# Performance work log

Hardware: AMD Instinct MI355X
Metric: run time of the kernel (lower is better)

## Reference

```python
import jax, jax.numpy as jnp
import numpy as np
from functools import partial

B, L, V = 64, 512, 20000
P, M = 150, 6          # total patterns, max pattern length
NEG = -1e9             # semiring zero (log-space)
END_STATES = np.repeat(np.array([3, 4, 5]), 50)  # pattern_len-1 per pattern


@jax.custom_vjp
def ste_heaviside(x):
    return (x > 0).astype(x.dtype)

def _ste_fwd(x):
    return ste_heaviside(x), None

def _ste_bwd(_, g):
    return (g,)  # straight-through identity (matches torch code path)

ste_heaviside.defvjp(_ste_fwd, _ste_bwd)


def setup_inputs() -> dict:
    key = jax.random.key(0)
    ks = jax.random.split(key, 8)
    return {
        "docs": jax.random.randint(ks[0], (B, L), 0, V),
        "doc_lens": jax.random.randint(ks[1], (B,), 1, L),
        "local_embeddings": jax.random.normal(ks[2], (300, V), jnp.float32),
        "diags": jax.random.normal(ks[3], (P * M, 300), jnp.float32) * 0.05,
        "bias": jax.random.normal(ks[4], (P * M, 1), jnp.float32) * 0.05,
        "wildcards": jax.random.normal(ks[5], (P, M - 1), jnp.float32) * 0.05,
        "ln_gamma": jnp.ones((P,), jnp.float32),
        "ln_beta": jnp.zeros((P,), jnp.float32),
        "linear_w": jax.random.normal(ks[6], (2, P), jnp.float32) * 0.05,
        "linear_b": jnp.zeros((2,), jnp.float32),
    }


def reference(docs, doc_lens, local_embeddings, diags, bias, wildcards,
              ln_gamma, ln_beta, linear_w, linear_b):
    end_states = jnp.asarray(END_STATES)                  # [P]
    pat_idx = jnp.arange(P)

    # transition matrices over local vocab, mapped into log-space semiring
    tm_vocab = jax.nn.log_sigmoid((diags @ local_embeddings + bias).T)  # [V, P*M]
    tm = tm_vocab[docs].reshape(B, L, P, M)               # [B,L,P,M]

    # wildcard transitions: semiring.times(one=0, log_sigmoid(wildcards))
    wild = jax.nn.log_sigmoid(wildcards)                  # [P, M-1]

    restart = jnp.zeros((B, P, 1), tm.dtype)              # semiring one
    hid0 = jnp.full((B, P, M), NEG, tm.dtype).at[:, :, 0].set(0.0)
    scores0 = jnp.full((B, P), NEG, tm.dtype)             # semiring zero

    def step(carry, inputs):
        hid, sc = carry
        t, tm_t = inputs                                  # tm_t: [B,P,M]
        main = jnp.concatenate([restart, hid[:, :, :-1] + tm_t[:, :, :-1]], axis=2)
        wildp = jnp.concatenate([restart, hid[:, :, :-1] + wild[None]], axis=2)
        hid = jnp.maximum(main, wildp)                    # semiring plus
        esv = hid[:, pat_idx, end_states]                 # [B,P]
        active = (doc_lens > t)[:, None]
        sc = jnp.where(active, jnp.maximum(sc, esv), sc)
        return (hid, sc), None

    xs = (jnp.arange(L), jnp.moveaxis(tm, 1, 0))          # [L], [L,B,P,M]
    (_, scores), _ = jax.lax.scan(step, (hid0, scores0), xs)

    scores = jnp.exp(scores)                              # from_semiring_to_outer
    mu = scores.mean(axis=-1, keepdims=True)
    var = scores.var(axis=-1, keepdims=True)
    norm = (scores - mu) * jax.lax.rsqrt(var + 1e-5) * ln_gamma + ln_beta
    binar = ste_heaviside(norm)
    return binar @ linear_w.T + linear_b
```

## Files before the change

### kernel.cpp

```cpp
#include <hip/hip_runtime.h>
#include <hip/hip_bf16.h>
#include <hip/hip_fp16.h>
#include <math.h>

#define B_   64
#define L_   512
#define V_   20000
#define P_   150
#define M_   6
#define KDIM 300
#define NOUT 750
#define CWS  752
#define NEGF (-1.0e9f)

#define BM 128
#define BN 128
#define BK 16
#define LDP 132

#define KP 320
#define NIT 10
#define NVG 157
#define NJ  6
#define TILE_U4 1024
#define SA 1024.0f
#define SB 16384.0f
#define INV24 (5.9604644775390625e-8f)

#define TCHUNK 32
#define NCHUNK (L_ / TCHUNK)
#define WARM   5
#define CS_STRIDE 160

typedef _Float16 f16x8 __attribute__((ext_vector_type(8)));
typedef float f32x16 __attribute__((ext_vector_type(16)));

__device__ __forceinline__ float logsigf(float x) {
    return fminf(x, 0.f) - log1pf(expf(-fabsf(x)));
}

__device__ __forceinline__ float logsigf_fast(float x) {
    return fminf(x, 0.f) - __logf(1.f + __expf(-fabsf(x)));
}

__device__ __forceinline__ void gload_lds16(const void* gp, void* lp) {
    __builtin_amdgcn_global_load_lds(
        (const __attribute__((address_space(1))) unsigned int*)gp,
        (__attribute__((address_space(3))) unsigned int*)lp, 16, 0, 0);
}


__global__ __launch_bounds__(256) void p12_split(
    const float* __restrict__ emb, const float* __restrict__ diags,
    uint4* __restrict__ a_t, uint4* __restrict__ b_t)
{
    __shared__ float T[64][132];
    const int t   = threadIdx.x;
    const int bid = blockIdx.x;

    if (bid < NVG * 5) {
        const int gx = bid % NVG;
        const int ky = bid / NVG;
        const int v0 = gx * 128;
        const int k0 = ky * 64;

        #pragma unroll
        for (int pass = 0; pass < 8; ++pass) {
            int flat = pass * 256 + t;
            int krow = flat >> 5;
            int c4   = (flat & 31) * 4;
            int kg   = k0 + krow;
            int v    = v0 + c4;
            float4 f = {0.f, 0.f, 0.f, 0.f};
            if (kg < KDIM && v + 3 < V_)
                f = *(const float4*)(emb + (size_t)kg * V_ + v);
            *(float4*)&T[krow][c4] = f;
        }
        __syncthreads();

        const int vv = t >> 1;
        const int kh = (t & 1) * 32;
        const int it = ky * 2 + (kh >> 5);
        const int v  = v0 + vv;
        if (v < V_) {
            union { ushort u[8]; uint4 q; } H[4], Lo[4];
            #pragma unroll
            for (int i = 0; i < 32; ++i) {
                float x = T[kh + i][vv] * SA;
                __half h = __float2half_rn(x);
                float rem = x - __half2float(h);
                H[i >> 3].u[i & 7]  = __half_as_ushort(h);
                Lo[i >> 3].u[i & 7] = __half_as_ushort(__float2half_rn(rem));
            }
            uint4* tile = a_t + ((size_t)gx * NIT + it) * TILE_U4;
            #pragma unroll
            for (int c = 0; c < 4; ++c) {
                tile[      c * 128 + vv] = H[c].q;
                tile[512 + c * 128 + vv] = Lo[c].q;
            }
        }
    } else {
        const int bidx = bid - NVG * 5;
        const int it   = bidx % NIT;
        const int j    = bidx / NIT;
        const int row  = t >> 1;
        const int qh   = (t & 1) * 2;
        const int n    = j * 128 + row;
        const bool nok = (n < NOUT);
        const int pm   = nok ? ((n / 5) * 6 + (n % 5)) : 0;
        uint4* tile = b_t + (size_t)bidx * TILE_U4;
        #pragma unroll
        for (int qq = 0; qq < 2; ++qq) {
            int q = qh + qq;
            union { ushort u[8]; uint4 v; } H, Lo;
            #pragma unroll
            for (int e = 0; e < 8; ++e) {
                int k = it * 32 + q * 8 + e;
                float x = (nok && k < KDIM) ? diags[(size_t)pm * KDIM + k] * SB : 0.f;
                __half h = __float2half_rn(x);
                float rem = x - __half2float(h);
                H.u[e]  = __half_as_ushort(h);
                Lo.u[e] = __half_as_ushort(__float2half_rn(rem));
            }
            tile[      q * 128 + row] = H.v;
            tile[512 + q * 128 + row] = Lo.v;
        }
    }
}

__global__ __launch_bounds__(256, 2) void k1m_gemm(
    const uint4* __restrict__ a_t, const uint4* __restrict__ b_t,
    const float* __restrict__ bias, const float* __restrict__ wildc,
    float* __restrict__ cw)
{
    const int bid  = blockIdx.x;
    const int xcd  = bid & 7;
    const int slot = bid >> 3;
    const int g    = xcd + 8 * (slot / 6);
    const int j    = slot % 6;
    if (g >= NVG) return;

    __shared__ uint4 sm[2][2048];
    const int t    = threadIdx.x;
    const int lane = t & 63;
    const int w    = t >> 6;
    const int wr   = w >> 1, wc = w & 1;
    const int v0   = g * 128;
    const int n0   = j * 128;

    const uint4* gsec = (w < 2)
        ? a_t + (size_t)g * NIT * TILE_U4 + w * 512
        : b_t + (size_t)j * NIT * TILE_U4 + (w - 2) * 512;

    const int fk16 = lane >> 5;
    const int fm   = lane & 31;

    f32x16 acc[2][2];
    #pragma unroll
    for (int i = 0; i < 2; ++i)
        #pragma unroll
        for (int jj = 0; jj < 2; ++jj)
            #pragma unroll
            for (int r = 0; r < 16; ++r) acc[i][jj][r] = 0.f;

    {
        const uint4* gp = gsec + lane;
        #pragma unroll
        for (int i = 0; i < 8; ++i)
            gload_lds16(gp + i * 64, &sm[0][w * 512 + i * 64 + lane]);
    }

    int cur = 0;
    for (int it = 0; it < NIT; ++it) {
        __syncthreads();

        if (it + 1 < NIT) {
            const uint4* gp = gsec + (size_t)(it + 1) * TILE_U4 + lane;
            #pragma unroll
            for (int i = 0; i < 8; ++i)
                gload_lds16(gp + i * 64, &sm[cur ^ 1][w * 512 + i * 64 + lane]);
        }

        const uint4* smc = sm[cur];
        #pragma unroll
        for (int s = 0; s < 2; ++s) {
            f16x8 A1[2], A2[2], B1[2], B2[2];
            const int q = s * 2 + fk16;
            #pragma unroll
            for (int ri = 0; ri < 2; ++ri) {
                A1[ri] = *(const f16x8*)&smc[(0 * 4 + q) * 128 + wr * 64 + ri * 32 + fm];
                A2[ri] = *(const f16x8*)&smc[(1 * 4 + q) * 128 + wr * 64 + ri * 32 + fm];
            }
            #pragma unroll
            for (int cj = 0; cj < 2; ++cj) {
                B1[cj] = *(const f16x8*)&smc[(2 * 4 + q) * 128 + wc * 64 + cj * 32 + fm];
                B2[cj] = *(const f16x8*)&smc[(3 * 4 + q) * 128 + wc * 64 + cj * 32 + fm];
            }
            #pragma unroll
            for (int ri = 0; ri < 2; ++ri)
                #pragma unroll
                for (int cj = 0; cj < 2; ++cj) {
                    acc[ri][cj] = __builtin_amdgcn_mfma_f32_32x32x16_f16(A1[ri], B1[cj], acc[ri][cj], 0, 0, 0);
                    acc[ri][cj] = __builtin_amdgcn_mfma_f32_32x32x16_f16(A1[ri], B2[cj], acc[ri][cj], 0, 0, 0);
                    acc[ri][cj] = __builtin_amdgcn_mfma_f32_32x32x16_f16(A2[ri], B1[cj], acc[ri][cj], 0, 0, 0);
                }
        }
        cur ^= 1;
    }

    float biasv[2], lwv[2]; int ncol[2]; bool nok[2];
    #pragma unroll
    for (int cj = 0; cj < 2; ++cj) {
        int n = n0 + wc * 64 + cj * 32 + fm;
        ncol[cj] = n;
        nok[cj]  = (n < NOUT);
        int nc = nok[cj] ? n : 0;
        int pm = (nc / 5) * 6 + (nc % 5);
        biasv[cj] = bias[pm];
        lwv[cj]   = logsigf_fast(wildc[nc]);
    }
    #pragma unroll
    for (int ri = 0; ri < 2; ++ri) {
        int vbase = v0 + wr * 64 + ri * 32 + 4 * fk16;
        #pragma unroll
        for (int cj = 0; cj < 2; ++cj) {
            if (!nok[cj]) continue;
            #pragma unroll
            for (int r = 0; r < 16; ++r) {
                int v = vbase + (r & 3) + 8 * (r >> 2);
                if (v < V_) {
                    float val = acc[ri][cj][r] * INV24 + biasv[cj];
                    cw[(size_t)v * CWS + ncol[cj]] = fmaxf(logsigf_fast(val), lwv[cj]);
                }
            }
        }
    }
}


__global__ __launch_bounds__(256) void k1_gemm_cw(
    const float* __restrict__ emb,
    const float* __restrict__ diags,
    const float* __restrict__ bias,
    const float* __restrict__ wildc,
    float* __restrict__ cw)
{
    __shared__ float As[BK][LDP];
    __shared__ float Bs[BK][LDP];

    const int tid = threadIdx.x;
    const int v0 = blockIdx.x * BM;
    const int n0 = blockIdx.y * BN;
    const int tx = tid & 15;
    const int ty = tid >> 4;

    float acc[8][8];
    #pragma unroll
    for (int i = 0; i < 8; ++i)
        #pragma unroll
        for (int j = 0; j < 8; ++j) acc[i][j] = 0.f;

    const int a_k = tid >> 4;
    const int a_v = (tid & 15) * 8;
    const int b_n   = tid >> 1;
    const int b_kof = (tid & 1) * 8;

    int  brow;
    bool bval;
    {
        int n = n0 + b_n;
        bval = (n < NOUT);
        brow = bval ? ((n / 5) * 6 + (n % 5)) : 0;
    }

    for (int k0 = 0; k0 < KDIM; k0 += BK) {
        {
            float4 f0 = {0,0,0,0}, f1 = {0,0,0,0};
            int k = k0 + a_k;
            if (k < KDIM) {
                const float* src = emb + (size_t)k * V_ + v0 + a_v;
                if (v0 + a_v + 3 < V_) f0 = *(const float4*)src;
                if (v0 + a_v + 7 < V_) f1 = *(const float4*)(src + 4);
            }
            *(float4*)&As[a_k][a_v]     = f0;
            *(float4*)&As[a_k][a_v + 4] = f1;
        }
        {
            float4 f = {0,0,0,0}, g = {0,0,0,0};
            if (bval) {
                const float* src = diags + (size_t)brow * KDIM + k0 + b_kof;
                if (k0 + b_kof + 3 < KDIM) f = *(const float4*)src;
                if (k0 + b_kof + 7 < KDIM) g = *(const float4*)(src + 4);
            }
            Bs[b_kof + 0][b_n] = f.x;
            Bs[b_kof + 1][b_n] = f.y;
            Bs[b_kof + 2][b_n] = f.z;
            Bs[b_kof + 3][b_n] = f.w;
            Bs[b_kof + 4][b_n] = g.x;
            Bs[b_kof + 5][b_n] = g.y;
            Bs[b_kof + 6][b_n] = g.z;
            Bs[b_kof + 7][b_n] = g.w;
        }
        __syncthreads();
        #pragma unroll
        for (int k = 0; k < BK; ++k) {
            float4 a0 = *(const float4*)&As[k][tx * 4];
            float4 a1 = *(const float4*)&As[k][64 + tx * 4];
            float4 b0 = *(const float4*)&Bs[k][ty * 8];
            float4 b1 = *(const float4*)&Bs[k][ty * 8 + 4];
            float av[8] = {a0.x, a0.y, a0.z, a0.w, a1.x, a1.y, a1.z, a1.w};
            float bv[8] = {b0.x, b0.y, b0.z, b0.w, b1.x, b1.y, b1.z, b1.w};
            #pragma unroll
            for (int i = 0; i < 8; ++i)
                #pragma unroll
                for (int j = 0; j < 8; ++j)
                    acc[i][j] = fmaf(av[i], bv[j], acc[i][j]);
        }
        __syncthreads();
    }

    float biasv[8], lwv[8];
    #pragma unroll
    for (int j = 0; j < 8; ++j) {
        int n  = n0 + ty * 8 + j;
        int nc = (n < NOUT) ? n : 0;
        int pm = (nc / 5) * 6 + (nc % 5);
        biasv[j] = bias[pm];
        lwv[j]   = logsigf(wildc[nc]);
    }
    #pragma unroll
    for (int i = 0; i < 8; ++i) {
        int v = v0 + ((i < 4) ? (tx * 4 + i) : (64 + tx * 4 + (i - 4)));
        if (v >= V_) continue;
        float r[8];
        #pragma unroll
        for (int j = 0; j < 8; ++j)
            r[j] = fmaxf(logsigf(acc[i][j] + biasv[j]), lwv[j]);
        float* dst = cw + (size_t)v * CWS + n0 + ty * 8;
        if (n0 + ty * 8     < NOUT) *(float4*)dst       = make_float4(r[0], r[1], r[2], r[3]);
        if (n0 + ty * 8 + 4 < NOUT) *(float4*)(dst + 4) = make_float4(r[4], r[5], r[6], r[7]);
    }
}


__global__ __launch_bounds__(192) void k2_scan(
    const int* __restrict__ docs,
    const int* __restrict__ doc_lens,
    const float* __restrict__ cw,
    float* __restrict__ cs)
{
    const int ci = blockIdx.x;
    const int b  = blockIdx.y;
    const int t0 = ci * TCHUNK;
    const int ts = (t0 >= WARM) ? (t0 - WARM) : 0;
    const int dl = doc_lens[b];
    const int te = min(t0 + TCHUNK, dl);
    const int nt = te - ts;

    __shared__ int   toks[TCHUNK + WARM];
    __shared__ float rows[3][768];

    const int t    = threadIdx.x;
    const int lane = t & 63;
    const int w    = t >> 6;

    if (t < TCHUNK + WARM) {
        int tt = ts + t;
        toks[t] = docs[b * L_ + min(tt, L_ - 1)];
    }
    __syncthreads();

    const int p      = t;
    const int e      = (p < 50) ? 3 : (p < 100) ? 4 : 5;
    const int warm_n = t0 - ts;
    float h1 = NEGF, h2 = NEGF, h3 = NEGF, h4 = NEGF, h5 = NEGF, sc = NEGF;

    const int nrounds = (nt > 0) ? (nt + 2) / 3 : 0;
    for (int r = 0; r < nrounds; ++r) {
        {
            int idx = min(3 * r + w, nt - 1);
            const char* rowp = (const char*)(cw + (size_t)toks[idx] * CWS);
            char* lbase = (char*)&rows[w][0];
            #pragma unroll
            for (int jj = 0; jj < 3; ++jj)
                gload_lds16(rowp + jj * 1024 + lane * 16,
                            lbase + jj * 1024 + lane * 16);
        }
        __syncthreads();

        #pragma unroll
        for (int u = 0; u < 3; ++u) {
            int i2 = 3 * r + u;
            if (i2 >= nt) break;
            if (p < P_) {
                const float* rp = &rows[u][p * 5];
                float c0 = rp[0], c1 = rp[1], c2 = rp[2], c3 = rp[3], c4 = rp[4];
                h5 = h4 + c4;
                h4 = h3 + c3;
                h3 = h2 + c2;
                h2 = h1 + c1;
                h1 = c0;
                if (i2 >= warm_n) {
                    float esv = (e == 3) ? h3 : (e == 4) ? h4 : h5;
                    sc = fmaxf(sc, esv);
                }
            }
        }
        __syncthreads();
    }
    if (p < P_) cs[(size_t)(b * NCHUNK + ci) * CS_STRIDE + p] = sc;
}

__device__ __forceinline__ float block_sum192(float v, volatile float* red, int tid) {
    #pragma unroll
    for (int off = 32; off > 0; off >>= 1) v += __shfl_down(v, off, 64);
    __syncthreads();
    if ((tid & 63) == 0) red[tid >> 6] = v;
    __syncthreads();
    return red[0] + red[1] + red[2];
}

__global__ __launch_bounds__(192) void k3_final(
    const float* __restrict__ cs,
    const float* __restrict__ gamma,
    const float* __restrict__ beta,
    const float* __restrict__ lw,
    const float* __restrict__ lb,
    float* __restrict__ out)
{
    __shared__ float red[3];
    const int b   = blockIdx.x;
    const int tid = threadIdx.x;
    float s = 0.f;
    if (tid < P_) {
        float m = NEGF;
        const float* row = cs + (size_t)b * NCHUNK * CS_STRIDE + tid;
        #pragma unroll
        for (int ci = 0; ci < NCHUNK; ++ci) m = fmaxf(m, row[ci * CS_STRIDE]);
        s = expf(m);
    }
    float mu = block_sum192(s, red, tid) * (1.f / P_);
    float d  = (tid < P_) ? (s - mu) : 0.f;
    float var = block_sum192(d * d, red, tid) * (1.f / P_);
    float bin = 0.f;
    if (tid < P_) {
        float norm = (s - mu) * rsqrtf(var + 1e-5f) * gamma[tid] + beta[tid];
        bin = (norm > 0.f) ? 1.f : 0.f;
    }
    float o0 = block_sum192((tid < P_) ? bin * lw[tid]      : 0.f, red, tid);
    float o1 = block_sum192((tid < P_) ? bin * lw[P_ + tid] : 0.f, red, tid);
    if (tid == 0) {
        out[b * 2 + 0] = o0 + lb[0];
        out[b * 2 + 1] = o1 + lb[1];
    }
}

extern "C" void kernel_launch(void* const* d_in, const int* in_sizes, int n_in,
                              void* d_out, int out_size, void* d_ws, size_t ws_size,
                              hipStream_t stream)
{
    const int*   docs  = (const int*)  d_in[0];
    const int*   dlens = (const int*)  d_in[1];
    const float* emb   = (const float*)d_in[2];
    const float* diags = (const float*)d_in[3];
    const float* bias  = (const float*)d_in[4];
    const float* wildc = (const float*)d_in[5];
    const float* gamma = (const float*)d_in[6];
    const float* beta  = (const float*)d_in[7];
    const float* lw    = (const float*)d_in[8];
    const float* lb    = (const float*)d_in[9];
    float* out = (float*)d_out;

    const size_t cw_b = (size_t)V_ * CWS * 4;
    const size_t cs_b = (size_t)B_ * NCHUNK * CS_STRIDE * 4;
    const size_t at_b = (size_t)NVG * NIT * TILE_U4 * 16;
    const size_t bt_b = (size_t)NJ  * NIT * TILE_U4 * 16;
    const size_t need = cw_b + cs_b + at_b + bt_b;

    char* base = (char*)d_ws;
    float* cw = (float*)base;
    float* cs = (float*)(base + cw_b);
    uint4* at = (uint4*)(base + cw_b + cs_b);
    uint4* bt = (uint4*)(base + cw_b + cs_b + at_b);

    if (ws_size >= need) {
        p12_split<<<NVG * 5 + NJ * NIT, 256, 0, stream>>>(emb, diags, at, bt);
        k1m_gemm<<<960, 256, 0, stream>>>(at, bt, bias, wildc, cw);
    } else {
        dim3 g1((V_ + BM - 1) / BM, (NOUT + BN - 1) / BN);
        k1_gemm_cw<<<g1, 256, 0, stream>>>(emb, diags, bias, wildc, cw);
    }

    dim3 g2(NCHUNK, B_);
    k2_scan<<<g2, 192, 0, stream>>>(docs, dlens, cw, cs);
    k3_final<<<B_, 192, 0, stream>>>(cs, gamma, beta, lw, lb, out);
}
```

Measured before the change: 151.3 us.

## Triple-buffer scan row loads with async prefetch and nontemporal table stores

The scan kernel now keeps three LDS buffers and prefetches the token rows two rounds ahead with async global-to-LDS loads. It waits on vmcnt and uses a single barrier per round instead of two, so gather latency overlaps with the recurrence. Separately, the GEMM epilogue writes the transition table with nontemporal stores to limit cache pollution. The cost is triple the LDS use in the scan, which may lower occupancy, and the barrier and vmcnt ordering must stay correct.

```diff
diff --git a/kernel.cpp b/kernel.cpp
--- a/kernel.cpp
+++ b/kernel.cpp
@@ -31,6 +31,7 @@
 #define NCHUNK (L_ / TCHUNK)
 #define WARM   5
 #define CS_STRIDE 160
+#define KVBUF 3
 
 typedef _Float16 f16x8 __attribute__((ext_vector_type(8)));
 typedef float f32x16 __attribute__((ext_vector_type(16)));
@@ -230,7 +231,9 @@
                 int v = vbase + (r & 3) + 8 * (r >> 2);
                 if (v < V_) {
                     float val = acc[ri][cj][r] * INV24 + biasv[cj];
-                    cw[(size_t)v * CWS + ncol[cj]] = fmaxf(logsigf_fast(val), lwv[cj]);
+                    __builtin_nontemporal_store(
+                        fmaxf(logsigf_fast(val), lwv[cj]),
+                        &cw[(size_t)v * CWS + ncol[cj]]);
                 }
             }
         }
@@ -358,7 +361,7 @@
     const int nt = te - ts;
 
     __shared__ int   toks[TCHUNK + WARM];
-    __shared__ float rows[3][768];
+    __shared__ float rows[KVBUF][3][768];
 
     const int t    = threadIdx.x;
     const int lane = t & 63;
@@ -376,24 +379,46 @@
     float h1 = NEGF, h2 = NEGF, h3 = NEGF, h4 = NEGF, h5 = NEGF, sc = NEGF;
 
     const int nrounds = (nt > 0) ? (nt + 2) / 3 : 0;
+
+    for (int r0 = 0; r0 < 2; ++r0) {
+        if (r0 >= nrounds) break;
+        int idx = min(3 * r0 + w, nt - 1);
+        const char* rowp = (const char*)(cw + (size_t)toks[idx] * CWS);
+        char* lbase = (char*)&rows[r0][w][0];
+        #pragma unroll
+        for (int jj = 0; jj < 3; ++jj)
+            gload_lds16(rowp + jj * 1024 + lane * 16,
+                        lbase + jj * 1024 + lane * 16);
+    }
+
+    int bufc = 0;
     for (int r = 0; r < nrounds; ++r) {
-        {
-            int idx = min(3 * r + w, nt - 1);
+        if (r + 1 < nrounds) {
+            asm volatile("s_waitcnt vmcnt(3)" ::: "memory");
+        } else {
+            asm volatile("s_waitcnt vmcnt(0)" ::: "memory");
+        }
+        __builtin_amdgcn_s_barrier();
+        asm volatile("" ::: "memory");
+
+        if (r + 2 < nrounds) {
+            int rn  = r + 2;
+            int idx = min(3 * rn + w, nt - 1);
             const char* rowp = (const char*)(cw + (size_t)toks[idx] * CWS);
-            char* lbase = (char*)&rows[w][0];
+            int bn = bufc + 2; if (bn >= KVBUF) bn -= KVBUF;
+            char* lbase = (char*)&rows[bn][w][0];
             #pragma unroll
             for (int jj = 0; jj < 3; ++jj)
                 gload_lds16(rowp + jj * 1024 + lane * 16,
                             lbase + jj * 1024 + lane * 16);
         }
-        __syncthreads();
 
         #pragma unroll
         for (int u = 0; u < 3; ++u) {
             int i2 = 3 * r + u;
             if (i2 >= nt) break;
             if (p < P_) {
-                const float* rp = &rows[u][p * 5];
+                const float* rp = &rows[bufc][u][p * 5];
                 float c0 = rp[0], c1 = rp[1], c2 = rp[2], c3 = rp[3], c4 = rp[4];
                 h5 = h4 + c4;
                 h4 = h3 + c3;
@@ -406,7 +431,7 @@
                 }
             }
         }
-        __syncthreads();
+        bufc = (bufc + 1 == KVBUF) ? 0 : bufc + 1;
     }
     if (p < P_) cs[(size_t)(b * NCHUNK + ci) * CS_STRIDE + p] = sc;
 }
```

Result: slower. 155.5 us (+2.8%).
